# Optimization experiments

Measured on AMD Instinct MI355X. Metric: run time of the kernel, lower is better.

The kernel has to match this reference:

```python
import jax, jax.numpy as jnp
import numpy as np

B, E, S, H = 4, 1024, 1024, 16
HD = E // H  # head_size = 64
MASK_VALUE = -1000000000.0
W_SCALE = 0.05  # keep pre-softmax logits moderate since original softmax is not max-stabilized


def setup_inputs() -> dict:
    key = jax.random.key(0)
    ks = jax.random.split(key, 7)
    queries = jax.random.normal(ks[0], (B, E, S), jnp.float32)
    keys = jax.random.normal(ks[1], (B, E, S), jnp.float32)
    values = jax.random.normal(ks[2], (B, E, S), jnp.float32)
    # causal multiplicative mask, broadcast over batch
    mask = jnp.broadcast_to(jnp.tril(jnp.ones((S, S), jnp.float32)), (B, S, S))
    Wq = jax.random.normal(ks[3], (H, HD, HD), jnp.float32) * W_SCALE
    Wk = jax.random.normal(ks[4], (H, HD, HD), jnp.float32) * W_SCALE
    Wv = jax.random.normal(ks[5], (H, HD, HD), jnp.float32) * W_SCALE
    Wf = jax.random.normal(ks[6], (E, E), jnp.float32) * W_SCALE
    return dict(queries=queries, keys=keys, values=values, mask=mask,
                Wq=Wq, Wk=Wk, Wv=Wv, Wf=Wf)


def reference(queries, keys, values, mask, Wq, Wk, Wv, Wf):
    # channels-first: [B, E, S] -> split embedding axis into heads: [B, H, HD, S]
    qh = queries.reshape(B, H, HD, S)
    kh = keys.reshape(B, H, HD, S)
    vh = values.reshape(B, H, HD, S)
    # per-head linear projections: W[h] @ x_slice, batched over heads
    q = jnp.einsum('hde,bhes->bhds', Wq, qh)
    k = jnp.einsum('hde,bhes->bhds', Wk, kh)
    v = jnp.einsum('hde,bhes->bhds', Wv, vh)
    # pre_softmax = Q^T @ K / sqrt(head_size)  -> [B, H, S, S]
    pre = jnp.einsum('bhds,bhdt->bhst', q, k) / jnp.sqrt(jnp.float32(HD))
    m = mask[:, None, :, :]  # broadcast mask over heads
    pre = pre * m + (m == 0).astype(jnp.float32) * MASK_VALUE
    # Faithful to original: exp / reduce_sum(axis=-1)[..., None, :]
    # i.e. post[b,h,i,j] = exp(pre[b,h,i,j]) / sum_t exp(pre[b,h,j,t])
    e = jnp.exp(pre)
    post = e / jnp.sum(e, axis=3)[:, :, None, :]
    # values @ post^T : out[b,h,d,i] = sum_j v[b,h,d,j] * post[b,h,i,j]
    out_h = jnp.einsum('bhdj,bhij->bhdi', v, post)
    pre_linear = out_h.reshape(B, E, S)  # concat heads along embedding axis
    return jnp.einsum('ef,bfs->bes', Wf, pre_linear)
```

## Files before the change

### kernel.cpp

```cpp
#include <hip/hip_runtime.h>
#include <hip/hip_bf16.h>
#include <stdint.h>

#define NB 4
#define NH 16
#define HDIM 64
#define NS 1024
#define NE 1024

typedef __bf16 bf16x8 __attribute__((ext_vector_type(8)));
typedef __bf16 bf16x2_t __attribute__((ext_vector_type(2)));
typedef float f32x4 __attribute__((ext_vector_type(4)));
typedef float f32x16 __attribute__((ext_vector_type(16)));
typedef unsigned int uint4v __attribute__((ext_vector_type(4)));
typedef unsigned int uint2v __attribute__((ext_vector_type(2)));
typedef unsigned short u16;

#if defined(__has_builtin)
#if __has_builtin(__builtin_amdgcn_global_load_lds)
#define HAVE_GLDS 1
#endif
#endif

__device__ __forceinline__ u16 f2bf(float f) {
  return __builtin_bit_cast(u16, (__bf16)f);
}
__device__ __forceinline__ unsigned pk2(float a, float b) {
  bf16x2_t v; v[0] = (__bf16)a; v[1] = (__bf16)b;
  return __builtin_bit_cast(unsigned, v);
}
__device__ __forceinline__ float fexp2(float x) {
#if defined(__has_builtin)
#if __has_builtin(__builtin_amdgcn_exp2f)
  return __builtin_amdgcn_exp2f(x);
#else
  return __expf(x * 0.69314718056f);
#endif
#else
  return __expf(x * 0.69314718056f);
#endif
}
__device__ __forceinline__ f32x4 mfma16(bf16x8 a, bf16x8 b, f32x4 c) {
  return __builtin_amdgcn_mfma_f32_16x16x32_bf16(a, b, c, 0, 0, 0);
}
__device__ __forceinline__ f32x16 mfma32(bf16x8 a, bf16x8 b, f32x16 c) {
  return __builtin_amdgcn_mfma_f32_32x32x16_bf16(a, b, c, 0, 0, 0);
}
__device__ __forceinline__ bf16x8 ld_bf8(const u16* p) {
  return __builtin_bit_cast(bf16x8, *(const uint4v*)p);
}
#ifdef HAVE_GLDS
__device__ __forceinline__ void gld16(const void* g, void* l) {
  __builtin_amdgcn_global_load_lds(
      (__attribute__((address_space(1))) void*)g,
      (__attribute__((address_space(3))) void*)l, 16, 0, 0);
}
#endif

#if defined(__has_builtin)
#if __has_builtin(__builtin_amdgcn_permlane32_swap)
#define HAVE_PLS 1
#endif
#endif
__device__ __forceinline__ uint2v plswap(unsigned a, unsigned b) {
#ifdef HAVE_PLS
  return __builtin_amdgcn_permlane32_swap(a, b, false, false);
#else
  unsigned asw = (unsigned)__shfl_xor((int)a, 32);
  unsigned bsw = (unsigned)__shfl_xor((int)b, 32);
  bool hi = (threadIdx.x & 32) != 0;
  uint2v r;
  r[0] = hi ? bsw : a;
  r[1] = hi ? b : asw;
  return r;
#endif
}

__global__ __launch_bounds__(256) void proj_kernel(
    const float* __restrict__ q_in, const float* __restrict__ k_in,
    const float* __restrict__ v_in, const float* __restrict__ Wq,
    const float* __restrict__ Wk, const float* __restrict__ Wv,
    const float* __restrict__ Wf,
    u16* __restrict__ qT, u16* __restrict__ kT, u16* __restrict__ vv,
    u16* __restrict__ Wf16)
{
  const int which = blockIdx.z;
  const int tid = threadIdx.x;

  if (which == 3) {
    int chunk = blockIdx.y * 4 + blockIdx.x;
    #pragma unroll
    for (int jj = 0; jj < 4; ++jj) {
      int i = chunk * 1024 + tid + 256 * jj;
      float4 f = ((const float4*)Wf)[i];
      uint2v p;
      p[0] = pk2(f.x, f.y);
      p[1] = pk2(f.z, f.w);
      ((uint2v*)Wf16)[i] = p;
    }
    return;
  }

  const int bh = blockIdx.y;
  const int b = bh >> 4, h = bh & 15;
  const int s0 = blockIdx.x * 256;
  const int w = tid >> 6, l = tid & 63, lr = l & 15, lg = l >> 4;

  const float* x = (which == 0) ? q_in : (which == 1) ? k_in : v_in;
  const float* W = ((which == 0) ? Wq : (which == 1) ? Wk : Wv) + h * 4096;
  const float wsc = (which == 0) ? 0.18033688f : 1.0f;

  __shared__ alignas(16) u16 xT[256][72];
  __shared__ alignas(16) u16 Wl[64][72];

  #pragma unroll
  for (int j = 0; j < 4; ++j) {
    int i = tid * 4 + j;
    int d = i >> 4;
    int e0 = (i & 15) * 4;
    float4 f = *(const float4*)(W + d * 64 + e0);
    uint2v p;
    p[0] = pk2(f.x * wsc, f.y * wsc);
    p[1] = pk2(f.z * wsc, f.w * wsc);
    *(uint2v*)&Wl[d][e0] = p;
  }
  {
    const float* xp = x + ((size_t)b * NE + h * 64) * NS + s0 + tid;
    #pragma unroll
    for (int j = 0; j < 8; ++j) {
      uint4v pk;
      #pragma unroll
      for (int q = 0; q < 4; ++q) {
        float f0 = xp[(size_t)(j * 8 + q * 2) * NS];
        float f1 = xp[(size_t)(j * 8 + q * 2 + 1) * NS];
        pk[q] = pk2(f0, f1);
      }
      *(uint4v*)&xT[tid][j * 8] = pk;
    }
  }
  __syncthreads();

  bf16x8 af[4][2];
  #pragma unroll
  for (int mt = 0; mt < 4; ++mt) {
    af[mt][0] = ld_bf8(&Wl[mt * 16 + lr][lg * 8]);
    af[mt][1] = ld_bf8(&Wl[mt * 16 + lr][32 + lg * 8]);
  }
  f32x4 acc[4][4] = {};
  #pragma unroll
  for (int nt = 0; nt < 4; ++nt) {
    bf16x8 b0 = ld_bf8(&xT[w * 64 + nt * 16 + lr][lg * 8]);
    bf16x8 b1 = ld_bf8(&xT[w * 64 + nt * 16 + lr][32 + lg * 8]);
    #pragma unroll
    for (int mt = 0; mt < 4; ++mt) {
      acc[mt][nt] = mfma16(af[mt][0], b0, acc[mt][nt]);
      acc[mt][nt] = mfma16(af[mt][1], b1, acc[mt][nt]);
    }
  }

  if (which < 2) {
    u16* o = ((which == 0) ? qT : kT) + (size_t)bh * NS * 64;
    #pragma unroll
    for (int mt = 0; mt < 4; ++mt)
      #pragma unroll
      for (int nt = 0; nt < 4; ++nt) {
        int s = s0 + w * 64 + nt * 16 + lr;
        int d = mt * 16 + lg * 4;
        uint2v p;
        p[0] = pk2(acc[mt][nt][0], acc[mt][nt][1]);
        p[1] = pk2(acc[mt][nt][2], acc[mt][nt][3]);
        *(uint2v*)(o + (size_t)s * 64 + d) = p;
      }
  } else {
    u16* o = vv + (size_t)bh * 64 * NS;
    #pragma unroll
    for (int mt = 0; mt < 4; ++mt)
      #pragma unroll
      for (int nt = 0; nt < 4; ++nt)
        #pragma unroll
        for (int jr = 0; jr < 4; ++jr) {
          int d = mt * 16 + lg * 4 + jr;
          int s = s0 + w * 64 + nt * 16 + lr;
          o[(size_t)d * NS + s] = f2bf(acc[mt][nt][jr]);
        }
  }
}

__global__ __launch_bounds__(512) void denom_kernel(
    const u16* __restrict__ qT, const u16* __restrict__ kT,
    float* __restrict__ l2rDg)
{
  const int wg = blockIdx.x;
  const int rt = 7 - (wg >> 6);
  const int bh = wg & 63;
  const int i0 = rt * 128;
  const int tid = threadIdx.x, w = tid >> 6, l = tid & 63, lr = l & 15, lg = l >> 4;
  __shared__ alignas(16) u16 klds[128][72];
  const u16* qb = qT + (size_t)bh * NS * 64;
  const u16* kb = kT + (size_t)bh * NS * 64;
  const int gi = i0 + w * 16 + lr;
  bf16x8 bq0 = ld_bf8(qb + (size_t)gi * 64 + lg * 8);
  bf16x8 bq1 = ld_bf8(qb + (size_t)gi * 64 + 32 + lg * 8);
  float den = 0.f;
  const int nkt = rt + 1;
  uint4v kreg[2];
  const int krow = tid >> 3, kcx = tid & 7;
  #pragma unroll
  for (int j = 0; j < 2; ++j)
    kreg[j] = *(const uint4v*)(kb + (size_t)(krow + j * 64) * 64 + kcx * 8);
  for (int t = 0; t < nkt; ++t) {
    __syncthreads();
    #pragma unroll
    for (int j = 0; j < 2; ++j)
      *(uint4v*)&klds[krow + j * 64][kcx * 8] = kreg[j];
    __syncthreads();
    const int t0 = t * 128;
    if (t + 1 < nkt) {
      #pragma unroll
      for (int j = 0; j < 2; ++j)
        kreg[j] = *(const uint4v*)(kb + (size_t)(t0 + 128 + krow + j * 64) * 64 + kcx * 8);
    }
    if (t + 1 < nkt) {
      #pragma unroll
      for (int mt = 0; mt < 8; ++mt) {
        bf16x8 a0 = ld_bf8(&klds[mt * 16 + lr][lg * 8]);
        bf16x8 a1 = ld_bf8(&klds[mt * 16 + lr][32 + lg * 8]);
        f32x4 z = {0.f, 0.f, 0.f, 0.f};
        f32x4 sc = mfma16(a0, bq0, z);
        sc = mfma16(a1, bq1, sc);
        den += fexp2(sc[0]) + fexp2(sc[1]) + fexp2(sc[2]) + fexp2(sc[3]);
      }
    } else {
      #pragma unroll
      for (int mt = 0; mt < 8; ++mt) {
        bf16x8 a0 = ld_bf8(&klds[mt * 16 + lr][lg * 8]);
        bf16x8 a1 = ld_bf8(&klds[mt * 16 + lr][32 + lg * 8]);
        f32x4 z = {0.f, 0.f, 0.f, 0.f};
        f32x4 sc = mfma16(a0, bq0, z);
        sc = mfma16(a1, bq1, sc);
        #pragma unroll
        for (int r = 0; r < 4; ++r) {
          int gt = t0 + mt * 16 + lg * 4 + r;
          den += (gt <= gi) ? fexp2(sc[r]) : 0.f;
        }
      }
    }
  }
  den += __shfl_xor(den, 16);
  den += __shfl_xor(den, 32);
  if (l < 16) l2rDg[(size_t)bh * NS + gi] = -__log2f(den);
}

__global__ __launch_bounds__(512) void attn_kernel(
    const u16* __restrict__ qT, const u16* __restrict__ kT,
    const u16* __restrict__ vv, const float* __restrict__ l2rDg,
    u16* __restrict__ X)
{
  const int wg = blockIdx.x;
  const int rt = 7 - (wg >> 6);
  const int bh = wg & 63;
  const int b = bh >> 4, h = bh & 15;
  const int i0 = rt * 128;
  const int tid = threadIdx.x, w = tid >> 6, l = tid & 63;
  const int q5 = l & 31, hf = l >> 5;
  const int qi = w >> 1, ki = w & 1;

  __shared__ alignas(16) unsigned char smem[2 * 64 * 72 * 2 * 2 + 2 * 64 * 4];
  typedef u16 (*tile_t)[64][72];
  tile_t klds = (tile_t)smem;
  tile_t vlds = (tile_t)(smem + 18432);
  float (*dlds)[64] = (float(*)[64])(smem + 36864);

  const u16* qb = qT + (size_t)bh * NS * 64;
  const u16* kb = kT + (size_t)bh * NS * 64;
  const u16* vb = vv + (size_t)bh * 64 * NS;
  const float* rb = l2rDg + (size_t)bh * NS;
  const int r0w = i0 + qi * 32;
  const int gi2 = r0w + q5;
  bf16x8 bq[4];
  #pragma unroll
  for (int dc = 0; dc < 4; ++dc)
    bq[dc] = ld_bf8(qb + (size_t)gi2 * 64 + dc * 16 + hf * 8);
  f32x16 acc[2] = {};
  const int nkt = 2 * rt + 2;
  uint4v kreg, vreg;
  float dreg = 0.f;
  const int crow = tid >> 3, ccx = tid & 7;
  kreg = *(const uint4v*)(kb + (size_t)crow * 64 + ccx * 8);
  vreg = *(const uint4v*)(vb + (size_t)crow * NS + ccx * 8);
  if (tid < 64) dreg = rb[tid];
  *(uint4v*)&klds[0][crow][ccx * 8] = kreg;
  *(uint4v*)&vlds[0][crow][ccx * 8] = vreg;
  if (tid < 64) dlds[0][tid] = dreg;
  __syncthreads();
  int p = 0;
  for (int t = 0; t < nkt; ++t) {
    const int t0 = t * 64;
    const bool more = (t + 1 < nkt);
    if (more) {
      const int t0n = t0 + 64;
      kreg = *(const uint4v*)(kb + (size_t)(t0n + crow) * 64 + ccx * 8);
      vreg = *(const uint4v*)(vb + (size_t)crow * NS + t0n + ccx * 8);
      if (tid < 64) dreg = rb[t0n + tid];
    }
    const int kb0 = t0 + ki * 32;
    if (kb0 <= r0w + 31) {
      const bool msk = (kb0 + 31 > r0w);
      bf16x8 ak0 = ld_bf8(&klds[p][ki * 32 + q5][0 * 16 + hf * 8]);
      bf16x8 ak1 = ld_bf8(&klds[p][ki * 32 + q5][1 * 16 + hf * 8]);
      bf16x8 ak2 = ld_bf8(&klds[p][ki * 32 + q5][2 * 16 + hf * 8]);
      bf16x8 ak3 = ld_bf8(&klds[p][ki * 32 + q5][3 * 16 + hf * 8]);
      f32x16 sa = {}, sb = {};
      sa = mfma32(ak0, bq[0], sa);
      sb = mfma32(ak2, bq[2], sb);
      sa = mfma32(ak1, bq[1], sa);
      sb = mfma32(ak3, bq[3], sb);
      f32x4 lv[4];
      #pragma unroll
      for (int g = 0; g < 4; ++g)
        lv[g] = *(const f32x4*)&dlds[p][ki * 32 + 4 * hf + 8 * g];
      float pe[16];
      if (!msk) {
        #pragma unroll
        for (int r = 0; r < 16; ++r)
          pe[r] = fexp2(sa[r] + sb[r] + lv[r >> 2][r & 3]);
      } else {
        #pragma unroll
        for (int r = 0; r < 16; ++r) {
          int key = kb0 + (r & 3) + 8 * (r >> 2) + 4 * hf;
          float e = fexp2(sa[r] + sb[r] + lv[r >> 2][r & 3]);
          pe[r] = (key <= gi2) ? e : 0.f;
        }
      }
      bf16x8 pa[2];
      #pragma unroll
      for (int f = 0; f < 2; ++f) {
        unsigned A0 = pk2(pe[8 * f + 0], pe[8 * f + 1]);
        unsigned A1 = pk2(pe[8 * f + 2], pe[8 * f + 3]);
        unsigned B0 = pk2(pe[8 * f + 4], pe[8 * f + 5]);
        unsigned B1 = pk2(pe[8 * f + 6], pe[8 * f + 7]);
        uint2v s0 = plswap(A0, B0);
        uint2v s1 = plswap(A1, B1);
        uint4v fw;
        fw[0] = s0[0]; fw[1] = s1[0]; fw[2] = s0[1]; fw[3] = s1[1];
        pa[f] = __builtin_bit_cast(bf16x8, fw);
      }
      __builtin_amdgcn_s_setprio(1);
      #pragma unroll
      for (int db = 0; db < 2; ++db) {
        #pragma unroll
        for (int f = 0; f < 2; ++f) {
          bf16x8 bv = ld_bf8(&vlds[p][db * 32 + q5][ki * 32 + f * 16 + hf * 8]);
          acc[db] = mfma32(pa[f], bv, acc[db]);
        }
      }
      __builtin_amdgcn_s_setprio(0);
    }
    if (more) {
      *(uint4v*)&klds[p ^ 1][crow][ccx * 8] = kreg;
      *(uint4v*)&vlds[p ^ 1][crow][ccx * 8] = vreg;
      if (tid < 64) dlds[p ^ 1][tid] = dreg;
      __syncthreads();
      p ^= 1;
    }
  }
  __syncthreads();
  float* flds = (float*)smem;
  if (ki == 1) {
    #pragma unroll
    for (int db = 0; db < 2; ++db)
      #pragma unroll
      for (int r = 0; r < 16; ++r) {
        int qrow = (r & 3) + 8 * (r >> 2) + 4 * hf;
        flds[(qi * 32 + qrow) * 64 + db * 32 + q5] = acc[db][r];
      }
  }
  __syncthreads();
  if (ki == 0) {
    u16* Xp = X + (size_t)b * NS * NE + h * 64;
    #pragma unroll
    for (int db = 0; db < 2; ++db)
      #pragma unroll
      for (int r = 0; r < 16; ++r) {
        int qrow = (r & 3) + 8 * (r >> 2) + 4 * hf;
        float v = acc[db][r] + flds[(qi * 32 + qrow) * 64 + db * 32 + q5];
        int srow = r0w + qrow;
        Xp[(size_t)srow * NE + db * 32 + q5] = f2bf(v);
      }
  }
}

__global__ __launch_bounds__(512) void final_gemm(
    const u16* __restrict__ Wf16, const u16* __restrict__ X,
    float* __restrict__ out)
{
  const int b = blockIdx.z;
  const int e0 = blockIdx.y * 128;
  const int s0 = blockIdx.x * 128;
  const int tid = threadIdx.x, w = tid >> 6, l = tid & 63, lr = l & 15, lg = l >> 4;
  const int wm = (w >> 2) * 64, wn = (w & 3) * 32;
  __shared__ alignas(16) u16 Ald[2][128][64];
  __shared__ alignas(16) u16 Bld[2][128][64];
  const u16* Xb = X + (size_t)b * NS * NE;
  f32x4 acc[4][2] = {};

  #define FG_ISSUE(p, k0)                                                     \
    {                                                                         \
      _Pragma("unroll")                                                       \
      for (int j = 0; j < 2; ++j) {                                           \
        int c = tid + 512 * j;                                                \
        int r = c >> 3;                                                       \
        int sc_ = ((c & 7) * 16) ^ ((r & 7) << 4);                            \
        const char* ga = (const char*)(Wf16 + (size_t)(e0 + r) * NE + (k0)) + sc_; \
        const char* gb = (const char*)(Xb + (size_t)(s0 + r) * NE + (k0)) + sc_;   \
        char* la = (char*)&Ald[p][0][0] + c * 16;                             \
        char* lb = (char*)&Bld[p][0][0] + c * 16;                             \
        STAGE16(ga, la);                                                      \
        STAGE16(gb, lb);                                                      \
      }                                                                       \
    }
#ifdef HAVE_GLDS
  #define STAGE16(g, l_) gld16((g), (l_))
#else
  #define STAGE16(g, l_) (*(uint4v*)(l_) = *(const uint4v*)(g))
#endif

  FG_ISSUE(0, 0);
  __syncthreads();
  for (int t = 0; t < 16; ++t) {
    const int p = t & 1;
    if (t < 15) FG_ISSUE(p ^ 1, (t + 1) * 64);
    __builtin_amdgcn_s_setprio(1);
    #pragma unroll
    for (int kk = 0; kk < 2; ++kk) {
      bf16x8 a[4], bb[2];
      #pragma unroll
      for (int mt = 0; mt < 4; ++mt) {
        int R = wm + mt * 16 + lr;
        a[mt] = ld_bf8((const u16*)((const char*)&Ald[p][R][0] +
                                    ((kk * 64 + lg * 16) ^ ((R & 7) << 4))));
      }
      #pragma unroll
      for (int nt = 0; nt < 2; ++nt) {
        int R = wn + nt * 16 + lr;
        bb[nt] = ld_bf8((const u16*)((const char*)&Bld[p][R][0] +
                                     ((kk * 64 + lg * 16) ^ ((R & 7) << 4))));
      }
      #pragma unroll
      for (int mt = 0; mt < 4; ++mt)
        #pragma unroll
        for (int nt = 0; nt < 2; ++nt)
          acc[mt][nt] = mfma16(a[mt], bb[nt], acc[mt][nt]);
    }
    __builtin_amdgcn_s_setprio(0);
    __syncthreads();
  }
  #pragma unroll
  for (int mt = 0; mt < 4; ++mt)
    #pragma unroll
    for (int nt = 0; nt < 2; ++nt) {
      int e = e0 + wm + mt * 16 + lg * 4;
      int s = s0 + wn + nt * 16 + lr;
      float* op = out + ((size_t)b * NE + e) * NS + s;
      op[0] = acc[mt][nt][0];
      op[NS] = acc[mt][nt][1];
      op[2 * NS] = acc[mt][nt][2];
      op[3 * NS] = acc[mt][nt][3];
    }
}

extern "C" void kernel_launch(void* const* d_in, const int* in_sizes, int n_in,
                              void* d_out, int out_size, void* d_ws, size_t ws_size,
                              hipStream_t stream) {
  (void)in_sizes; (void)n_in; (void)out_size; (void)ws_size;
  const float* q_in = (const float*)d_in[0];
  const float* k_in = (const float*)d_in[1];
  const float* v_in = (const float*)d_in[2];
  const float* Wq = (const float*)d_in[4];
  const float* Wk = (const float*)d_in[5];
  const float* Wv = (const float*)d_in[6];
  const float* Wf = (const float*)d_in[7];

  u16* qT = (u16*)d_ws;
  u16* kT = qT + (size_t)NB * NH * NS * HDIM;
  u16* vv = kT + (size_t)NB * NH * NS * HDIM;
  u16* X  = vv + (size_t)NB * NH * HDIM * NS;
  u16* Wf16 = X + (size_t)NB * NS * NE;
  float* l2rD = (float*)(Wf16 + (size_t)NE * NE);

  proj_kernel<<<dim3(4, 64, 4), 256, 0, stream>>>(q_in, k_in, v_in, Wq, Wk, Wv,
                                                  Wf, qT, kT, vv, Wf16);
  denom_kernel<<<dim3(512), 512, 0, stream>>>(qT, kT, l2rD);
  attn_kernel<<<dim3(512), 512, 0, stream>>>(qT, kT, vv, l2rD, X);
  final_gemm<<<dim3(8, 8, 4), 512, 0, stream>>>(Wf16, X, (float*)d_out);
}
```

Baseline: 71.07 us.

## Fuse denominator and attention kernels with inter-block flag synchronization

Merges the column-denominator pass and the attention pass into one kernel. Each block first computes the denominators for its 128-row tile, publishes them with a release flag, then runs attention and spin-waits on the flags of earlier tiles before it reads their denominators. This removes one kernel launch and the gap between kernels, and lets attention overlap with other blocks' denominator work. In exchange it adds a memset, spin-waits, and a deadlock risk if blocks that publish needed flags are not resident; it also doubles the LDS allocation, sets launch bounds to 4 blocks, and merges the split QK accumulators into one.

```diff
diff --git a/kernel.cpp b/kernel.cpp
--- a/kernel.cpp
+++ b/kernel.cpp
@@ -186,75 +186,10 @@
   }
 }
 
-__global__ __launch_bounds__(512) void denom_kernel(
+__global__ __launch_bounds__(512, 4) void dattn_kernel(
     const u16* __restrict__ qT, const u16* __restrict__ kT,
-    float* __restrict__ l2rDg)
-{
-  const int wg = blockIdx.x;
-  const int rt = 7 - (wg >> 6);
-  const int bh = wg & 63;
-  const int i0 = rt * 128;
-  const int tid = threadIdx.x, w = tid >> 6, l = tid & 63, lr = l & 15, lg = l >> 4;
-  __shared__ alignas(16) u16 klds[128][72];
-  const u16* qb = qT + (size_t)bh * NS * 64;
-  const u16* kb = kT + (size_t)bh * NS * 64;
-  const int gi = i0 + w * 16 + lr;
-  bf16x8 bq0 = ld_bf8(qb + (size_t)gi * 64 + lg * 8);
-  bf16x8 bq1 = ld_bf8(qb + (size_t)gi * 64 + 32 + lg * 8);
-  float den = 0.f;
-  const int nkt = rt + 1;
-  uint4v kreg[2];
-  const int krow = tid >> 3, kcx = tid & 7;
-  #pragma unroll
-  for (int j = 0; j < 2; ++j)
-    kreg[j] = *(const uint4v*)(kb + (size_t)(krow + j * 64) * 64 + kcx * 8);
-  for (int t = 0; t < nkt; ++t) {
-    __syncthreads();
-    #pragma unroll
-    for (int j = 0; j < 2; ++j)
-      *(uint4v*)&klds[krow + j * 64][kcx * 8] = kreg[j];
-    __syncthreads();
-    const int t0 = t * 128;
-    if (t + 1 < nkt) {
-      #pragma unroll
-      for (int j = 0; j < 2; ++j)
-        kreg[j] = *(const uint4v*)(kb + (size_t)(t0 + 128 + krow + j * 64) * 64 + kcx * 8);
-    }
-    if (t + 1 < nkt) {
-      #pragma unroll
-      for (int mt = 0; mt < 8; ++mt) {
-        bf16x8 a0 = ld_bf8(&klds[mt * 16 + lr][lg * 8]);
-        bf16x8 a1 = ld_bf8(&klds[mt * 16 + lr][32 + lg * 8]);
-        f32x4 z = {0.f, 0.f, 0.f, 0.f};
-        f32x4 sc = mfma16(a0, bq0, z);
-        sc = mfma16(a1, bq1, sc);
-        den += fexp2(sc[0]) + fexp2(sc[1]) + fexp2(sc[2]) + fexp2(sc[3]);
-      }
-    } else {
-      #pragma unroll
-      for (int mt = 0; mt < 8; ++mt) {
-        bf16x8 a0 = ld_bf8(&klds[mt * 16 + lr][lg * 8]);
-        bf16x8 a1 = ld_bf8(&klds[mt * 16 + lr][32 + lg * 8]);
-        f32x4 z = {0.f, 0.f, 0.f, 0.f};
-        f32x4 sc = mfma16(a0, bq0, z);
-        sc = mfma16(a1, bq1, sc);
-        #pragma unroll
-        for (int r = 0; r < 4; ++r) {
-          int gt = t0 + mt * 16 + lg * 4 + r;
-          den += (gt <= gi) ? fexp2(sc[r]) : 0.f;
-        }
-      }
-    }
-  }
-  den += __shfl_xor(den, 16);
-  den += __shfl_xor(den, 32);
-  if (l < 16) l2rDg[(size_t)bh * NS + gi] = -__log2f(den);
-}
-
-__global__ __launch_bounds__(512) void attn_kernel(
-    const u16* __restrict__ qT, const u16* __restrict__ kT,
-    const u16* __restrict__ vv, const float* __restrict__ l2rDg,
-    u16* __restrict__ X)
+    const u16* __restrict__ vv, float* __restrict__ l2rDg,
+    unsigned* __restrict__ flags, u16* __restrict__ X)
 {
   const int wg = blockIdx.x;
   const int rt = 7 - (wg >> 6);
@@ -262,131 +197,201 @@
   const int b = bh >> 4, h = bh & 15;
   const int i0 = rt * 128;
   const int tid = threadIdx.x, w = tid >> 6, l = tid & 63;
-  const int q5 = l & 31, hf = l >> 5;
-  const int qi = w >> 1, ki = w & 1;
-
-  __shared__ alignas(16) unsigned char smem[2 * 64 * 72 * 2 * 2 + 2 * 64 * 4];
-  typedef u16 (*tile_t)[64][72];
-  tile_t klds = (tile_t)smem;
-  tile_t vlds = (tile_t)(smem + 18432);
-  float (*dlds)[64] = (float(*)[64])(smem + 36864);
+
+  __shared__ alignas(16) unsigned char smem[37376 * 2];
 
   const u16* qb = qT + (size_t)bh * NS * 64;
   const u16* kb = kT + (size_t)bh * NS * 64;
   const u16* vb = vv + (size_t)bh * 64 * NS;
-  const float* rb = l2rDg + (size_t)bh * NS;
-  const int r0w = i0 + qi * 32;
-  const int gi2 = r0w + q5;
-  bf16x8 bq[4];
-  #pragma unroll
-  for (int dc = 0; dc < 4; ++dc)
-    bq[dc] = ld_bf8(qb + (size_t)gi2 * 64 + dc * 16 + hf * 8);
-  f32x16 acc[2] = {};
-  const int nkt = 2 * rt + 2;
-  uint4v kreg, vreg;
-  float dreg = 0.f;
-  const int crow = tid >> 3, ccx = tid & 7;
-  kreg = *(const uint4v*)(kb + (size_t)crow * 64 + ccx * 8);
-  vreg = *(const uint4v*)(vb + (size_t)crow * NS + ccx * 8);
-  if (tid < 64) dreg = rb[tid];
-  *(uint4v*)&klds[0][crow][ccx * 8] = kreg;
-  *(uint4v*)&vlds[0][crow][ccx * 8] = vreg;
-  if (tid < 64) dlds[0][tid] = dreg;
-  __syncthreads();
-  int p = 0;
-  for (int t = 0; t < nkt; ++t) {
-    const int t0 = t * 64;
-    const bool more = (t + 1 < nkt);
-    if (more) {
-      const int t0n = t0 + 64;
-      kreg = *(const uint4v*)(kb + (size_t)(t0n + crow) * 64 + ccx * 8);
-      vreg = *(const uint4v*)(vb + (size_t)crow * NS + t0n + ccx * 8);
-      if (tid < 64) dreg = rb[t0n + tid];
-    }
-    const int kb0 = t0 + ki * 32;
-    if (kb0 <= r0w + 31) {
-      const bool msk = (kb0 + 31 > r0w);
-      bf16x8 ak0 = ld_bf8(&klds[p][ki * 32 + q5][0 * 16 + hf * 8]);
-      bf16x8 ak1 = ld_bf8(&klds[p][ki * 32 + q5][1 * 16 + hf * 8]);
-      bf16x8 ak2 = ld_bf8(&klds[p][ki * 32 + q5][2 * 16 + hf * 8]);
-      bf16x8 ak3 = ld_bf8(&klds[p][ki * 32 + q5][3 * 16 + hf * 8]);
-      f32x16 sa = {}, sb = {};
-      sa = mfma32(ak0, bq[0], sa);
-      sb = mfma32(ak2, bq[2], sb);
-      sa = mfma32(ak1, bq[1], sa);
-      sb = mfma32(ak3, bq[3], sb);
-      f32x4 lv[4];
-      #pragma unroll
-      for (int g = 0; g < 4; ++g)
-        lv[g] = *(const f32x4*)&dlds[p][ki * 32 + 4 * hf + 8 * g];
-      float pe[16];
-      if (!msk) {
-        #pragma unroll
-        for (int r = 0; r < 16; ++r)
-          pe[r] = fexp2(sa[r] + sb[r] + lv[r >> 2][r & 3]);
+  float* rbw = l2rDg + (size_t)bh * NS;
+  unsigned* fl = flags + bh * 8;
+
+  {
+    u16 (*klds)[72] = (u16(*)[72])smem;
+    const int lr = l & 15, lg = l >> 4;
+    const int gi = i0 + w * 16 + lr;
+    bf16x8 bq0 = ld_bf8(qb + (size_t)gi * 64 + lg * 8);
+    bf16x8 bq1 = ld_bf8(qb + (size_t)gi * 64 + 32 + lg * 8);
+    float den = 0.f;
+    const int nkt = rt + 1;
+    uint4v kreg[2];
+    const int krow = tid >> 3, kcx = tid & 7;
+    #pragma unroll
+    for (int j = 0; j < 2; ++j)
+      kreg[j] = *(const uint4v*)(kb + (size_t)(krow + j * 64) * 64 + kcx * 8);
+    for (int t = 0; t < nkt; ++t) {
+      __syncthreads();
+      #pragma unroll
+      for (int j = 0; j < 2; ++j)
+        *(uint4v*)&klds[krow + j * 64][kcx * 8] = kreg[j];
+      __syncthreads();
+      const int t0 = t * 128;
+      if (t + 1 < nkt) {
+        #pragma unroll
+        for (int j = 0; j < 2; ++j)
+          kreg[j] = *(const uint4v*)(kb + (size_t)(t0 + 128 + krow + j * 64) * 64 + kcx * 8);
+      }
+      if (t + 1 < nkt) {
+        #pragma unroll
+        for (int mt = 0; mt < 8; ++mt) {
+          bf16x8 a0 = ld_bf8(&klds[mt * 16 + lr][lg * 8]);
+          bf16x8 a1 = ld_bf8(&klds[mt * 16 + lr][32 + lg * 8]);
+          f32x4 z = {0.f, 0.f, 0.f, 0.f};
+          f32x4 sc = mfma16(a0, bq0, z);
+          sc = mfma16(a1, bq1, sc);
+          den += fexp2(sc[0]) + fexp2(sc[1]) + fexp2(sc[2]) + fexp2(sc[3]);
+        }
       } else {
         #pragma unroll
+        for (int mt = 0; mt < 8; ++mt) {
+          bf16x8 a0 = ld_bf8(&klds[mt * 16 + lr][lg * 8]);
+          bf16x8 a1 = ld_bf8(&klds[mt * 16 + lr][32 + lg * 8]);
+          f32x4 z = {0.f, 0.f, 0.f, 0.f};
+          f32x4 sc = mfma16(a0, bq0, z);
+          sc = mfma16(a1, bq1, sc);
+          #pragma unroll
+          for (int r = 0; r < 4; ++r) {
+            int gt = t0 + mt * 16 + lg * 4 + r;
+            den += (gt <= gi) ? fexp2(sc[r]) : 0.f;
+          }
+        }
+      }
+    }
+    den += __shfl_xor(den, 16);
+    den += __shfl_xor(den, 32);
+    if (l < 16) rbw[gi] = -__log2f(den);
+    __syncthreads();
+    if (tid == 0)
+      __hip_atomic_store(&fl[rt], 1u, __ATOMIC_RELEASE, __HIP_MEMORY_SCOPE_AGENT);
+  }
+
+  {
+    const int q5 = l & 31, hf = l >> 5;
+    const int qi = w >> 1, ki = w & 1;
+    typedef u16 (*tile_t)[64][72];
+    tile_t klds = (tile_t)smem;
+    tile_t vlds = (tile_t)(smem + 18432);
+    float (*dlds)[64] = (float(*)[64])(smem + 36864);
+    const float* rb = l2rDg + (size_t)bh * NS;
+    const int r0w = i0 + qi * 32;
+    const int gi2 = r0w + q5;
+    bf16x8 bq[4];
+    #pragma unroll
+    for (int dc = 0; dc < 4; ++dc)
+      bq[dc] = ld_bf8(qb + (size_t)gi2 * 64 + dc * 16 + hf * 8);
+    f32x16 acc[2] = {};
+    const int nkt = 2 * rt + 2;
+    uint4v kreg, vreg;
+    float dreg = 0.f;
+    const int crow = tid >> 3, ccx = tid & 7;
+    kreg = *(const uint4v*)(kb + (size_t)crow * 64 + ccx * 8);
+    vreg = *(const uint4v*)(vb + (size_t)crow * NS + ccx * 8);
+    if (tid < 64) {
+      while (__hip_atomic_load(&fl[0], __ATOMIC_ACQUIRE, __HIP_MEMORY_SCOPE_AGENT) == 0)
+        __builtin_amdgcn_s_sleep(8);
+      dreg = rb[tid];
+    }
+    *(uint4v*)&klds[0][crow][ccx * 8] = kreg;
+    *(uint4v*)&vlds[0][crow][ccx * 8] = vreg;
+    if (tid < 64) dlds[0][tid] = dreg;
+    __syncthreads();
+    int p = 0;
+    for (int t = 0; t < nkt; ++t) {
+      const int t0 = t * 64;
+      const bool more = (t + 1 < nkt);
+      if (more) {
+        const int t0n = t0 + 64;
+        kreg = *(const uint4v*)(kb + (size_t)(t0n + crow) * 64 + ccx * 8);
+        vreg = *(const uint4v*)(vb + (size_t)crow * NS + t0n + ccx * 8);
+        if (tid < 64) {
+          while (__hip_atomic_load(&fl[(t + 1) >> 1], __ATOMIC_ACQUIRE,
+                                   __HIP_MEMORY_SCOPE_AGENT) == 0)
+            __builtin_amdgcn_s_sleep(8);
+          dreg = rb[t0n + tid];
+        }
+      }
+      const int kb0 = t0 + ki * 32;
+      if (kb0 <= r0w + 31) {
+        const bool msk = (kb0 + 31 > r0w);
+        f32x16 sc = {};
+        #pragma unroll
+        for (int dc = 0; dc < 4; ++dc) {
+          bf16x8 ak = ld_bf8(&klds[p][ki * 32 + q5][dc * 16 + hf * 8]);
+          sc = mfma32(ak, bq[dc], sc);
+        }
+        f32x4 lv[4];
+        #pragma unroll
+        for (int g = 0; g < 4; ++g)
+          lv[g] = *(const f32x4*)&dlds[p][ki * 32 + 4 * hf + 8 * g];
+        float pe[16];
+        if (!msk) {
+          #pragma unroll
+          for (int r = 0; r < 16; ++r)
+            pe[r] = fexp2(sc[r] + lv[r >> 2][r & 3]);
+        } else {
+          #pragma unroll
+          for (int r = 0; r < 16; ++r) {
+            int key = kb0 + (r & 3) + 8 * (r >> 2) + 4 * hf;
+            float e = fexp2(sc[r] + lv[r >> 2][r & 3]);
+            pe[r] = (key <= gi2) ? e : 0.f;
+          }
+        }
+        bf16x8 pa[2];
+        #pragma unroll
+        for (int f = 0; f < 2; ++f) {
+          unsigned A0 = pk2(pe[8 * f + 0], pe[8 * f + 1]);
+          unsigned A1 = pk2(pe[8 * f + 2], pe[8 * f + 3]);
+          unsigned B0 = pk2(pe[8 * f + 4], pe[8 * f + 5]);
+          unsigned B1 = pk2(pe[8 * f + 6], pe[8 * f + 7]);
+          uint2v s0 = plswap(A0, B0);
+          uint2v s1 = plswap(A1, B1);
+          uint4v fw;
+          fw[0] = s0[0]; fw[1] = s1[0]; fw[2] = s0[1]; fw[3] = s1[1];
+          pa[f] = __builtin_bit_cast(bf16x8, fw);
+        }
+        __builtin_amdgcn_s_setprio(1);
+        #pragma unroll
+        for (int db = 0; db < 2; ++db) {
+          #pragma unroll
+          for (int f = 0; f < 2; ++f) {
+            bf16x8 bv = ld_bf8(&vlds[p][db * 32 + q5][ki * 32 + f * 16 + hf * 8]);
+            acc[db] = mfma32(pa[f], bv, acc[db]);
+          }
+        }
+        __builtin_amdgcn_s_setprio(0);
+      }
+      if (more) {
+        *(uint4v*)&klds[p ^ 1][crow][ccx * 8] = kreg;
+        *(uint4v*)&vlds[p ^ 1][crow][ccx * 8] = vreg;
+        if (tid < 64) dlds[p ^ 1][tid] = dreg;
+        __syncthreads();
+        p ^= 1;
+      }
+    }
+    __syncthreads();
+    float* flds = (float*)smem;
+    if (ki == 1) {
+      #pragma unroll
+      for (int db = 0; db < 2; ++db)
+        #pragma unroll
         for (int r = 0; r < 16; ++r) {
-          int key = kb0 + (r & 3) + 8 * (r >> 2) + 4 * hf;
-          float e = fexp2(sa[r] + sb[r] + lv[r >> 2][r & 3]);
-          pe[r] = (key <= gi2) ? e : 0.f;
-        }
-      }
-      bf16x8 pa[2];
-      #pragma unroll
-      for (int f = 0; f < 2; ++f) {
-        unsigned A0 = pk2(pe[8 * f + 0], pe[8 * f + 1]);
-        unsigned A1 = pk2(pe[8 * f + 2], pe[8 * f + 3]);
-        unsigned B0 = pk2(pe[8 * f + 4], pe[8 * f + 5]);
-        unsigned B1 = pk2(pe[8 * f + 6], pe[8 * f + 7]);
-        uint2v s0 = plswap(A0, B0);
-        uint2v s1 = plswap(A1, B1);
-        uint4v fw;
-        fw[0] = s0[0]; fw[1] = s1[0]; fw[2] = s0[1]; fw[3] = s1[1];
-        pa[f] = __builtin_bit_cast(bf16x8, fw);
-      }
-      __builtin_amdgcn_s_setprio(1);
-      #pragma unroll
-      for (int db = 0; db < 2; ++db) {
-        #pragma unroll
-        for (int f = 0; f < 2; ++f) {
-          bf16x8 bv = ld_bf8(&vlds[p][db * 32 + q5][ki * 32 + f * 16 + hf * 8]);
-          acc[db] = mfma32(pa[f], bv, acc[db]);
-        }
-      }
-      __builtin_amdgcn_s_setprio(0);
-    }
-    if (more) {
-      *(uint4v*)&klds[p ^ 1][crow][ccx * 8] = kreg;
-      *(uint4v*)&vlds[p ^ 1][crow][ccx * 8] = vreg;
-      if (tid < 64) dlds[p ^ 1][tid] = dreg;
-      __syncthreads();
-      p ^= 1;
-    }
-  }
-  __syncthreads();
-  float* flds = (float*)smem;
-  if (ki == 1) {
-    #pragma unroll
-    for (int db = 0; db < 2; ++db)
-      #pragma unroll
-      for (int r = 0; r < 16; ++r) {
-        int qrow = (r & 3) + 8 * (r >> 2) + 4 * hf;
-        flds[(qi * 32 + qrow) * 64 + db * 32 + q5] = acc[db][r];
-      }
-  }
-  __syncthreads();
-  if (ki == 0) {
-    u16* Xp = X + (size_t)b * NS * NE + h * 64;
-    #pragma unroll
-    for (int db = 0; db < 2; ++db)
-      #pragma unroll
-      for (int r = 0; r < 16; ++r) {
-        int qrow = (r & 3) + 8 * (r >> 2) + 4 * hf;
-        float v = acc[db][r] + flds[(qi * 32 + qrow) * 64 + db * 32 + q5];
-        int srow = r0w + qrow;
-        Xp[(size_t)srow * NE + db * 32 + q5] = f2bf(v);
-      }
+          int qrow = (r & 3) + 8 * (r >> 2) + 4 * hf;
+          flds[(qi * 32 + qrow) * 64 + db * 32 + q5] = acc[db][r];
+        }
+    }
+    __syncthreads();
+    if (ki == 0) {
+      u16* Xp = X + (size_t)b * NS * NE + h * 64;
+      #pragma unroll
+      for (int db = 0; db < 2; ++db)
+        #pragma unroll
+        for (int r = 0; r < 16; ++r) {
+          int qrow = (r & 3) + 8 * (r >> 2) + 4 * hf;
+          float v = acc[db][r] + flds[(qi * 32 + qrow) * 64 + db * 32 + q5];
+          int srow = r0w + qrow;
+          Xp[(size_t)srow * NE + db * 32 + q5] = f2bf(v);
+        }
+    }
   }
 }
 
@@ -487,10 +492,11 @@
   u16* X  = vv + (size_t)NB * NH * HDIM * NS;
   u16* Wf16 = X + (size_t)NB * NS * NE;
   float* l2rD = (float*)(Wf16 + (size_t)NE * NE);
+  unsigned* flags = (unsigned*)(l2rD + (size_t)NB * NH * NS);
 
   proj_kernel<<<dim3(4, 64, 4), 256, 0, stream>>>(q_in, k_in, v_in, Wq, Wk, Wv,
                                                   Wf, qT, kT, vv, Wf16);
-  denom_kernel<<<dim3(512), 512, 0, stream>>>(qT, kT, l2rD);
-  attn_kernel<<<dim3(512), 512, 0, stream>>>(qT, kT, vv, l2rD, X);
+  hipMemsetAsync(flags, 0, 512 * sizeof(unsigned), stream);
+  dattn_kernel<<<dim3(512), 512, 0, stream>>>(qT, kT, vv, l2rD, flags, X);
   final_gemm<<<dim3(8, 8, 4), 512, 0, stream>>>(Wf16, X, (float*)d_out);
 }
```

After: 103.1 us. 1.45x slower.
